# Performance work log

Hardware: AMD Instinct MI355X
Metric: run time of the kernel (lower is better)

## Reference

```python
import jax, jax.numpy as jnp
import numpy as np

N_NODES = 10000
N_EDGES = 640000
IN_CH = 128
OUT_CH = 128


def setup_inputs() -> dict:
    key = jax.random.key(0)
    k1, k2, k3, k4 = jax.random.split(key, 4)
    x = jax.random.normal(k1, (N_NODES, IN_CH), dtype=jnp.float32)
    edge_index = jax.random.randint(k2, (2, N_EDGES), 0, N_NODES, dtype=jnp.int64)
    # nn.Linear(2*in_channels, out_channels): weight [out, 2*in], bias [out]
    bound = 1.0 / np.sqrt(2 * IN_CH)
    W = jax.random.uniform(k3, (OUT_CH, 2 * IN_CH), dtype=jnp.float32, minval=-bound, maxval=bound)
    b = jax.random.uniform(k4, (OUT_CH,), dtype=jnp.float32, minval=-bound, maxval=bound)
    return {"x": x, "W": W, "b": b, "edge_index": edge_index}


def reference(x, W, b, edge_index):
    # PyG convention: edge_index[0] = source j, edge_index[1] = target i
    src, dst = edge_index[0], edge_index[1]
    x_i = x[dst]                      # [E, C] target features
    x_j = x[src]                      # [E, C] source features
    feat = jnp.concatenate([x_i, x_j - x_i], axis=-1)  # [E, 2C]
    msg = feat @ W.T + b              # [E, out]
    out = jax.ops.segment_max(msg, dst, num_segments=x.shape[0])  # [N, out]
    # isolated nodes: PyG scatter-max yields 0, segment_max yields -inf
    return jnp.where(jnp.isfinite(out), out, 0.0)
```

## Files before the change

### kernel.cpp

```cpp
#include <hip/hip_runtime.h>
#include <math.h>

#define N_CH 128
#define NB_MAX 512
#define BIN_CHUNK 4096
#define BIN_T 512

__global__ __launch_bounds__(256) void prep_kernel(const float* __restrict__ W,
                                                   float* __restrict__ V1,
                                                   float* __restrict__ V2,
                                                   int* __restrict__ binCount,
                                                   int nb) {
    int i = blockIdx.x * 256 + threadIdx.x;
    if (i < N_CH * N_CH) {
        int k = i >> 7, o = i & 127;
        float w1 = W[o * 256 + k];
        float w2 = W[o * 256 + 128 + k];
        V1[i] = w1 - w2;
        V2[i] = w2;
    }
    if (i < nb) binCount[i] = 0;
}

__global__ __launch_bounds__(256) void gemm_kernel(const float* __restrict__ x,
                                                   const float* __restrict__ V1,
                                                   const float* __restrict__ V2,
                                                   const float* __restrict__ bias,
                                                   float* __restrict__ A,
                                                   unsigned short* __restrict__ Bh,
                                                   int n_nodes) {
    __shared__ float xs[32][N_CH];
    const int n0 = blockIdx.x * 32;
    const int tid = threadIdx.x;

    if (n0 + 32 <= n_nodes) {
        const float4* xg = (const float4*)(x + (size_t)n0 * N_CH);
        float4* xsv = (float4*)&xs[0][0];
        #pragma unroll
        for (int i = 0; i < 4; ++i) xsv[tid + i * 256] = xg[tid + i * 256];
    } else {
        for (int i = tid; i < 32 * N_CH; i += 256) {
            int n = n0 + (i >> 7);
            (&xs[0][0])[i] = (n < n_nodes) ? x[(size_t)n * N_CH + (i & 127)] : 0.f;
        }
    }
    __syncthreads();

    const int o  = tid & 127;
    const int nh = tid >> 7;
    const float bo = bias[o];
    float acc1[16], acc2[16];
    #pragma unroll
    for (int i = 0; i < 16; ++i) { acc1[i] = 0.f; acc2[i] = 0.f; }

    const float* xrow = &xs[nh * 16][0];
    for (int k4 = 0; k4 < N_CH; k4 += 4) {
        float w1[4], w2[4];
        #pragma unroll
        for (int j = 0; j < 4; ++j) {
            w1[j] = V1[(k4 + j) * N_CH + o];
            w2[j] = V2[(k4 + j) * N_CH + o];
        }
        #pragma unroll
        for (int i = 0; i < 16; ++i) {
            float4 xv = *(const float4*)&xrow[i * N_CH + k4];
            acc1[i] = fmaf(xv.x, w1[0], acc1[i]); acc2[i] = fmaf(xv.x, w2[0], acc2[i]);
            acc1[i] = fmaf(xv.y, w1[1], acc1[i]); acc2[i] = fmaf(xv.y, w2[1], acc2[i]);
            acc1[i] = fmaf(xv.z, w1[2], acc1[i]); acc2[i] = fmaf(xv.z, w2[2], acc2[i]);
            acc1[i] = fmaf(xv.w, w1[3], acc1[i]); acc2[i] = fmaf(xv.w, w2[3], acc2[i]);
        }
    }

    #pragma unroll
    for (int i = 0; i < 16; ++i) {
        int n = n0 + nh * 16 + i;
        if (n < n_nodes) {
            A[(size_t)n * N_CH + o] = acc1[i] + bo;
            unsigned int bits = __float_as_uint(acc2[i]);
            unsigned int r = (bits + 0x7FFFu + ((bits >> 16) & 1u)) >> 16;
            Bh[(size_t)n * N_CH + o] = (unsigned short)r;
        }
    }
}

__global__ __launch_bounds__(256) void bhist_kernel(const int* __restrict__ dst,
                                                    int* __restrict__ binCount,
                                                    int n_edges, int nb) {
    __shared__ int h[NB_MAX];
    const int tid = threadIdx.x;
    for (int i = tid; i < nb; i += 256) h[i] = 0;
    __syncthreads();
    const int base = blockIdx.x * BIN_CHUNK;
    const int cnt = min(BIN_CHUNK, n_edges - base);
    for (int j = tid; j < cnt; j += 256)
        atomicAdd(&h[dst[base + j] >> 5], 1);
    __syncthreads();
    for (int i = tid; i < nb; i += 256)
        if (h[i]) atomicAdd(&binCount[i], h[i]);
}

__global__ __launch_bounds__(512) void bscan_kernel(const int* __restrict__ binCount,
                                                    int* __restrict__ binOff,
                                                    int* __restrict__ binCursor,
                                                    int nb) {
    __shared__ int t[512];
    const int tid = threadIdx.x;
    int v = (tid < nb) ? binCount[tid] : 0;
    t[tid] = v;
    __syncthreads();
    #pragma unroll
    for (int off = 1; off < 512; off <<= 1) {
        int u = (tid >= off) ? t[tid - off] : 0;
        __syncthreads();
        t[tid] += u;
        __syncthreads();
    }
    if (tid < nb) {
        int excl = t[tid] - v;
        binOff[tid] = excl;
        binCursor[tid] = excl;
    }
    if (tid == 0) binOff[nb] = t[nb - 1];
}

__global__ __launch_bounds__(BIN_T) void bin_kernel(const int* __restrict__ src,
                                                    const int* __restrict__ dst,
                                                    int* __restrict__ binCursor,
                                                    unsigned int* __restrict__ binned,
                                                    int n_edges, int nb) {
    __shared__ unsigned int   lpk[BIN_CHUNK];
    __shared__ unsigned short lbk[BIN_CHUNK];
    __shared__ int sc[512];
    __shared__ int lhist[NB_MAX], lexcl[NB_MAX], lcur[NB_MAX], bbase[NB_MAX];

    const int tid = threadIdx.x;
    const int base = blockIdx.x * BIN_CHUNK;
    const int cnt = min(BIN_CHUNK, n_edges - base);

    for (int i = tid; i < nb; i += BIN_T) lhist[i] = 0;
    __syncthreads();

    unsigned int vreg[BIN_CHUNK / BIN_T];
    unsigned short breg[BIN_CHUNK / BIN_T];
    int nloc = 0;
    for (int j = tid; j < cnt; j += BIN_T) {
        int s = src[base + j];
        int d = dst[base + j];
        int b = d >> 5;
        vreg[nloc] = ((unsigned int)(d & 31) << 14) | (unsigned int)s;
        breg[nloc] = (unsigned short)b;
        ++nloc;
        atomicAdd(&lhist[b], 1);
    }
    __syncthreads();

    int v = (tid < nb) ? lhist[tid] : 0;
    sc[tid] = v;
    __syncthreads();
    #pragma unroll
    for (int off = 1; off < 512; off <<= 1) {
        int u = (tid >= off) ? sc[tid - off] : 0;
        __syncthreads();
        sc[tid] += u;
        __syncthreads();
    }
    if (tid < nb) {
        int excl = sc[tid] - v;
        lexcl[tid] = excl;
        lcur[tid] = excl;
    }
    __syncthreads();

    for (int k = 0; k < nloc; ++k) {
        int b = breg[k];
        int p = atomicAdd(&lcur[b], 1);
        lpk[p] = vreg[k];
        lbk[p] = (unsigned short)b;
    }
    __syncthreads();

    for (int b = tid; b < nb; b += BIN_T) {
        int c = lhist[b];
        if (c) bbase[b] = atomicAdd(&binCursor[b], c);
    }
    __syncthreads();

    for (int i = tid; i < cnt; i += BIN_T) {
        int b = lbk[i];
        binned[bbase[b] + (i - lexcl[b])] = lpk[i];
    }
}

__global__ __launch_bounds__(256) void build_kernel(const unsigned int* __restrict__ binned,
                                                    const int* __restrict__ binOff,
                                                    int* __restrict__ offsets,
                                                    int* __restrict__ eidx,
                                                    int n_nodes, int nb) {
    __shared__ int lhist[32], lexcl[33], lcur[32];
    const int b = blockIdx.x;
    const int tid = threadIdx.x;
    const int rbeg = binOff[b], rend = binOff[b + 1];

    if (tid < 32) { lhist[tid] = 0; lcur[tid] = 0; }
    __syncthreads();
    for (int i = rbeg + tid; i < rend; i += 256)
        atomicAdd(&lhist[binned[i] >> 14], 1);
    __syncthreads();
    if (tid == 0) {
        int s = 0;
        for (int k = 0; k < 32; ++k) { lexcl[k] = s; s += lhist[k]; }
        lexcl[32] = s;
    }
    __syncthreads();
    if (tid < 32) {
        int n = b * 32 + tid;
        if (n < n_nodes) offsets[n] = rbeg + lexcl[tid];
    }
    if (b == nb - 1 && tid == 0) offsets[n_nodes] = rend;
    for (int i = rbeg + tid; i < rend; i += 256) {
        unsigned int w = binned[i];
        int d5 = (int)(w >> 14);
        int r = atomicAdd(&lcur[d5], 1);
        eidx[rbeg + lexcl[d5] + r] = (int)(w & 16383u);
    }
}

__global__ __launch_bounds__(256) void gather_kernel(
        const float* __restrict__ A,
        const unsigned int* __restrict__ Bh2,
        const int* __restrict__ offsets,
        const int* __restrict__ eidx,
        float* __restrict__ out,
        int n_nodes) {
    __shared__ int sidx[4][64];
    const int g = threadIdx.x >> 6;
    const int l = threadIdx.x & 63;
    const int n = blockIdx.x * 4 + g;
    if (n >= n_nodes) return;
    const int beg = offsets[n], end = offsets[n + 1];

    float mlo[8], mhi[8];
    #pragma unroll
    for (int i = 0; i < 8; ++i) { mlo[i] = -INFINITY; mhi[i] = -INFINITY; }

    for (int base = beg; base < end; base += 64) {
        int p = base + l;
        if (p < end) sidx[g][l] = eidx[p];
        int cnt = min(64, end - base);
        int q = 0;
        for (; q + 8 <= cnt; q += 8) {
            unsigned int w[8];
            #pragma unroll
            for (int i = 0; i < 8; ++i)
                w[i] = Bh2[(size_t)sidx[g][q + i] * 64 + l];
            #pragma unroll
            for (int i = 0; i < 8; ++i) {
                mlo[i] = fmaxf(mlo[i], __uint_as_float(w[i] << 16));
                mhi[i] = fmaxf(mhi[i], __uint_as_float(w[i] & 0xFFFF0000u));
            }
        }
        for (; q < cnt; ++q) {
            unsigned int w = Bh2[(size_t)sidx[g][q] * 64 + l];
            mlo[0] = fmaxf(mlo[0], __uint_as_float(w << 16));
            mhi[0] = fmaxf(mhi[0], __uint_as_float(w & 0xFFFF0000u));
        }
    }

    float lo = mlo[0], hi = mhi[0];
    #pragma unroll
    for (int i = 1; i < 8; ++i) { lo = fmaxf(lo, mlo[i]); hi = fmaxf(hi, mhi[i]); }

    float2 r = make_float2(0.f, 0.f);
    if (end > beg) {
        float2 a = *(const float2*)(A + (size_t)n * N_CH + 2 * l);
        r.x = a.x + lo;
        r.y = a.y + hi;
    }
    *(float2*)(out + (size_t)n * N_CH + 2 * l) = r;
}

extern "C" void kernel_launch(void* const* d_in, const int* in_sizes, int n_in,
                              void* d_out, int out_size, void* d_ws, size_t ws_size,
                              hipStream_t stream) {
    const float* x = (const float*)d_in[0];
    const float* W = (const float*)d_in[1];
    const float* b = (const float*)d_in[2];
    const int*   ei = (const int*)d_in[3];

    const int n_nodes = in_sizes[0] / N_CH;
    const int n_edges = in_sizes[3] / 2;
    const int nb = (n_nodes + 31) >> 5;
    const int* src = ei;
    const int* dst = ei + n_edges;
    float* out = (float*)d_out;

    char* ws = (char*)d_ws;
    size_t off = 0;
    auto alloc = [&](size_t bytes) -> void* {
        void* p = ws + off;
        off += (bytes + 255) & ~(size_t)255;
        return p;
    };
    float* V1        = (float*)alloc((size_t)N_CH * N_CH * 4);
    float* V2        = (float*)alloc((size_t)N_CH * N_CH * 4);
    float* A         = (float*)alloc((size_t)n_nodes * N_CH * 4);
    unsigned short* Bh = (unsigned short*)alloc((size_t)n_nodes * N_CH * 2);
    int*   binCount  = (int*)alloc((size_t)nb * 4);
    int*   binOff    = (int*)alloc((size_t)(nb + 1) * 4);
    int*   binCursor = (int*)alloc((size_t)nb * 4);
    unsigned int* binned = (unsigned int*)alloc((size_t)n_edges * 4);
    int*   offsets   = (int*)alloc((size_t)(n_nodes + 1) * 4);
    int*   eidx      = (int*)alloc((size_t)n_edges * 4);
    (void)ws_size; (void)n_in; (void)out_size;

    const int nbin_blocks = (n_edges + BIN_CHUNK - 1) / BIN_CHUNK;

    prep_kernel <<<(N_CH * N_CH + 255) / 256, 256, 0, stream>>>(W, V1, V2, binCount, nb);
    gemm_kernel <<<(n_nodes + 31) / 32, 256, 0, stream>>>(x, V1, V2, b, A, Bh, n_nodes);
    bhist_kernel<<<nbin_blocks, 256, 0, stream>>>(dst, binCount, n_edges, nb);
    bscan_kernel<<<1, 512, 0, stream>>>(binCount, binOff, binCursor, nb);
    bin_kernel  <<<nbin_blocks, BIN_T, 0, stream>>>(src, dst, binCursor, binned, n_edges, nb);
    build_kernel<<<nb, 256, 0, stream>>>(binned, binOff, offsets, eidx, n_nodes, nb);
    gather_kernel<<<(n_nodes + 3) / 4, 256, 0, stream>>>(A, (const unsigned int*)Bh, offsets, eidx, out, n_nodes);
}
```

Before: 138.5 us.

## Replace global bin-cursor atomics with per-block histograms and in-block scans

The W-prep and the bin histogram are merged into one kernel that writes per-block bin counts, so the separate global histogram and scan kernels go away. The bin kernel now gets each block's global offsets by summing the per-block counts itself and running warp-shuffle scans. This gives a deterministic, stable ordering and drops the global cursor atomics. Packing the full destination into the binned word removes the separate bin-id array, loads are vectorised as int4, and the build kernel uses per-wave histograms to cut LDS atomic contention. In exchange, every bin block redundantly reads all nblk×nb counts (about 157×313 ints).

```diff
diff --git a/kernel.cpp b/kernel.cpp
--- a/kernel.cpp
+++ b/kernel.cpp
@@ -6,20 +6,67 @@
 #define BIN_CHUNK 4096
 #define BIN_T 512
 
-__global__ __launch_bounds__(256) void prep_kernel(const float* __restrict__ W,
-                                                   float* __restrict__ V1,
-                                                   float* __restrict__ V2,
-                                                   int* __restrict__ binCount,
-                                                   int nb) {
-    int i = blockIdx.x * 256 + threadIdx.x;
-    if (i < N_CH * N_CH) {
-        int k = i >> 7, o = i & 127;
-        float w1 = W[o * 256 + k];
-        float w2 = W[o * 256 + 128 + k];
-        V1[i] = w1 - w2;
-        V2[i] = w2;
-    }
-    if (i < nb) binCount[i] = 0;
+__device__ __forceinline__ int block_excl_scan512(int v, int tid, int* wsums) {
+    __syncthreads();
+    const int lane = tid & 63, w = tid >> 6;
+    int inc = v;
+    #pragma unroll
+    for (int i = 1; i < 64; i <<= 1) {
+        int t = __shfl_up(inc, i, 64);
+        if (lane >= i) inc += t;
+    }
+    if (lane == 63) wsums[w] = inc;
+    __syncthreads();
+    if (w == 0) {
+        int s = (lane < 8) ? wsums[lane] : 0;
+        #pragma unroll
+        for (int i = 1; i < 8; i <<= 1) {
+            int t = __shfl_up(s, i, 64);
+            if (lane >= i) s += t;
+        }
+        if (lane < 8) wsums[lane] = s;
+    }
+    __syncthreads();
+    int base = (w > 0) ? wsums[w - 1] : 0;
+    return base + inc - v;
+}
+
+__global__ __launch_bounds__(BIN_T) void preph_kernel(const float* __restrict__ W,
+                                                      const int* __restrict__ dst,
+                                                      float* __restrict__ V1,
+                                                      float* __restrict__ V2,
+                                                      int* __restrict__ binCountPB,
+                                                      int n_edges, int nb, int nblk) {
+    const int tid = threadIdx.x;
+    if ((int)blockIdx.x == nblk) {
+        for (int i = tid; i < N_CH * N_CH; i += BIN_T) {
+            int k = i >> 7, o = i & 127;
+            float w1 = W[o * 256 + k];
+            float w2 = W[o * 256 + 128 + k];
+            V1[i] = w1 - w2;
+            V2[i] = w2;
+        }
+        return;
+    }
+    __shared__ int h[NB_MAX];
+    for (int i = tid; i < nb; i += BIN_T) h[i] = 0;
+    __syncthreads();
+    const int base = blockIdx.x * BIN_CHUNK;
+    const int cnt = min(BIN_CHUNK, n_edges - base);
+    for (int j0 = tid * 4; j0 < cnt; j0 += BIN_T * 4) {
+        if (j0 + 3 < cnt) {
+            int4 d = *(const int4*)(dst + base + j0);
+            atomicAdd(&h[d.x >> 5], 1);
+            atomicAdd(&h[d.y >> 5], 1);
+            atomicAdd(&h[d.z >> 5], 1);
+            atomicAdd(&h[d.w >> 5], 1);
+        } else {
+            for (int j = j0; j < cnt; ++j) atomicAdd(&h[dst[base + j] >> 5], 1);
+        }
+    }
+    __syncthreads();
+    for (int i = tid; i < nb; i += BIN_T)
+        binCountPB[blockIdx.x * nb + i] = h[i];
 }
 
 __global__ __launch_bounds__(256) void gemm_kernel(const float* __restrict__ x,
@@ -83,111 +130,73 @@
     }
 }
 
-__global__ __launch_bounds__(256) void bhist_kernel(const int* __restrict__ dst,
-                                                    int* __restrict__ binCount,
-                                                    int n_edges, int nb) {
-    __shared__ int h[NB_MAX];
-    const int tid = threadIdx.x;
-    for (int i = tid; i < nb; i += 256) h[i] = 0;
-    __syncthreads();
-    const int base = blockIdx.x * BIN_CHUNK;
-    const int cnt = min(BIN_CHUNK, n_edges - base);
-    for (int j = tid; j < cnt; j += 256)
-        atomicAdd(&h[dst[base + j] >> 5], 1);
-    __syncthreads();
-    for (int i = tid; i < nb; i += 256)
-        if (h[i]) atomicAdd(&binCount[i], h[i]);
-}
-
-__global__ __launch_bounds__(512) void bscan_kernel(const int* __restrict__ binCount,
-                                                    int* __restrict__ binOff,
-                                                    int* __restrict__ binCursor,
-                                                    int nb) {
-    __shared__ int t[512];
-    const int tid = threadIdx.x;
-    int v = (tid < nb) ? binCount[tid] : 0;
-    t[tid] = v;
-    __syncthreads();
-    #pragma unroll
-    for (int off = 1; off < 512; off <<= 1) {
-        int u = (tid >= off) ? t[tid - off] : 0;
-        __syncthreads();
-        t[tid] += u;
-        __syncthreads();
-    }
-    if (tid < nb) {
-        int excl = t[tid] - v;
-        binOff[tid] = excl;
-        binCursor[tid] = excl;
-    }
-    if (tid == 0) binOff[nb] = t[nb - 1];
-}
-
 __global__ __launch_bounds__(BIN_T) void bin_kernel(const int* __restrict__ src,
                                                     const int* __restrict__ dst,
-                                                    int* __restrict__ binCursor,
+                                                    const int* __restrict__ binCountPB,
+                                                    int* __restrict__ binOff,
                                                     unsigned int* __restrict__ binned,
-                                                    int n_edges, int nb) {
-    __shared__ unsigned int   lpk[BIN_CHUNK];
-    __shared__ unsigned short lbk[BIN_CHUNK];
-    __shared__ int sc[512];
-    __shared__ int lhist[NB_MAX], lexcl[NB_MAX], lcur[NB_MAX], bbase[NB_MAX];
+                                                    int n_edges, int nb, int nblk) {
+    __shared__ unsigned int lpk[BIN_CHUNK];
+    __shared__ int gbase[NB_MAX];
+    __shared__ int lexcl[NB_MAX];
+    __shared__ int lcur[NB_MAX];
+    __shared__ int gOff[NB_MAX];
+    __shared__ int wsums[8];
 
     const int tid = threadIdx.x;
-    const int base = blockIdx.x * BIN_CHUNK;
+    const int bid = blockIdx.x;
+    const int base = bid * BIN_CHUNK;
     const int cnt = min(BIN_CHUNK, n_edges - base);
 
-    for (int i = tid; i < nb; i += BIN_T) lhist[i] = 0;
-    __syncthreads();
+    int tot = 0, pre = 0, own = 0;
+    if (tid < nb) {
+        for (int j = 0; j < nblk; ++j) {
+            int c = binCountPB[j * nb + tid];
+            tot += c;
+            if (j < bid) pre += c;
+            if (j == bid) own = c;
+        }
+    }
+    int offT = block_excl_scan512(tot, tid, wsums);
+    if (tid < nb) gOff[tid] = offT;
+    int offO = block_excl_scan512(own, tid, wsums);
+    if (tid < nb) {
+        lexcl[tid] = offO;
+        lcur[tid] = offO;
+        gbase[tid] = offT + pre;
+    }
+    if (bid == 0 && tid == 0) binOff[nb] = n_edges;
+    __syncthreads();
+    if (bid == 0) {
+        for (int i = tid; i < nb; i += BIN_T) binOff[i] = gOff[i];
+    }
 
     unsigned int vreg[BIN_CHUNK / BIN_T];
-    unsigned short breg[BIN_CHUNK / BIN_T];
     int nloc = 0;
-    for (int j = tid; j < cnt; j += BIN_T) {
-        int s = src[base + j];
-        int d = dst[base + j];
-        int b = d >> 5;
-        vreg[nloc] = ((unsigned int)(d & 31) << 14) | (unsigned int)s;
-        breg[nloc] = (unsigned short)b;
-        ++nloc;
-        atomicAdd(&lhist[b], 1);
-    }
-    __syncthreads();
-
-    int v = (tid < nb) ? lhist[tid] : 0;
-    sc[tid] = v;
-    __syncthreads();
-    #pragma unroll
-    for (int off = 1; off < 512; off <<= 1) {
-        int u = (tid >= off) ? sc[tid - off] : 0;
-        __syncthreads();
-        sc[tid] += u;
-        __syncthreads();
-    }
-    if (tid < nb) {
-        int excl = sc[tid] - v;
-        lexcl[tid] = excl;
-        lcur[tid] = excl;
-    }
-    __syncthreads();
-
+    for (int j0 = tid * 4; j0 < cnt; j0 += BIN_T * 4) {
+        if (j0 + 3 < cnt) {
+            int4 s4 = *(const int4*)(src + base + j0);
+            int4 d4 = *(const int4*)(dst + base + j0);
+            vreg[nloc++] = ((unsigned int)d4.x << 14) | (unsigned int)s4.x;
+            vreg[nloc++] = ((unsigned int)d4.y << 14) | (unsigned int)s4.y;
+            vreg[nloc++] = ((unsigned int)d4.z << 14) | (unsigned int)s4.z;
+            vreg[nloc++] = ((unsigned int)d4.w << 14) | (unsigned int)s4.w;
+        } else {
+            for (int j = j0; j < cnt; ++j)
+                vreg[nloc++] = ((unsigned int)dst[base + j] << 14) | (unsigned int)src[base + j];
+        }
+    }
     for (int k = 0; k < nloc; ++k) {
-        int b = breg[k];
+        int b = (int)(vreg[k] >> 19);
         int p = atomicAdd(&lcur[b], 1);
         lpk[p] = vreg[k];
-        lbk[p] = (unsigned short)b;
-    }
-    __syncthreads();
-
-    for (int b = tid; b < nb; b += BIN_T) {
-        int c = lhist[b];
-        if (c) bbase[b] = atomicAdd(&binCursor[b], c);
     }
     __syncthreads();
 
     for (int i = tid; i < cnt; i += BIN_T) {
-        int b = lbk[i];
-        binned[bbase[b] + (i - lexcl[b])] = lpk[i];
+        unsigned int w = lpk[i];
+        int b = (int)(w >> 19);
+        binned[gbase[b] + (i - lexcl[b])] = w;
     }
 }
 
@@ -196,32 +205,46 @@
                                                     int* __restrict__ offsets,
                                                     int* __restrict__ eidx,
                                                     int n_nodes, int nb) {
-    __shared__ int lhist[32], lexcl[33], lcur[32];
+    __shared__ int whist[4][32];
+    __shared__ int lexcl[33];
     const int b = blockIdx.x;
     const int tid = threadIdx.x;
+    const int w = tid >> 6;
     const int rbeg = binOff[b], rend = binOff[b + 1];
 
-    if (tid < 32) { lhist[tid] = 0; lcur[tid] = 0; }
+    if (tid < 128) ((int*)whist)[tid] = 0;
     __syncthreads();
     for (int i = rbeg + tid; i < rend; i += 256)
-        atomicAdd(&lhist[binned[i] >> 14], 1);
+        atomicAdd(&whist[w][(binned[i] >> 14) & 31], 1);
     __syncthreads();
     if (tid == 0) {
         int s = 0;
-        for (int k = 0; k < 32; ++k) { lexcl[k] = s; s += lhist[k]; }
+        #pragma unroll
+        for (int k = 0; k < 32; ++k) {
+            lexcl[k] = s;
+            s += whist[0][k] + whist[1][k] + whist[2][k] + whist[3][k];
+        }
         lexcl[32] = s;
     }
     __syncthreads();
     if (tid < 32) {
+        int basec = lexcl[tid];
+        #pragma unroll
+        for (int ww = 0; ww < 4; ++ww) {
+            int c = whist[ww][tid];
+            whist[ww][tid] = basec;
+            basec += c;
+        }
         int n = b * 32 + tid;
         if (n < n_nodes) offsets[n] = rbeg + lexcl[tid];
     }
     if (b == nb - 1 && tid == 0) offsets[n_nodes] = rend;
+    __syncthreads();
     for (int i = rbeg + tid; i < rend; i += 256) {
-        unsigned int w = binned[i];
-        int d5 = (int)(w >> 14);
-        int r = atomicAdd(&lcur[d5], 1);
-        eidx[rbeg + lexcl[d5] + r] = (int)(w & 16383u);
+        unsigned int wd = binned[i];
+        int v = (int)((wd >> 14) & 31);
+        int r = atomicAdd(&whist[w][v], 1);
+        eidx[rbeg + r] = (int)(wd & 16383u);
     }
 }
 
@@ -301,25 +324,22 @@
         off += (bytes + 255) & ~(size_t)255;
         return p;
     };
-    float* V1        = (float*)alloc((size_t)N_CH * N_CH * 4);
-    float* V2        = (float*)alloc((size_t)N_CH * N_CH * 4);
-    float* A         = (float*)alloc((size_t)n_nodes * N_CH * 4);
+    const int nblk = (n_edges + BIN_CHUNK - 1) / BIN_CHUNK;
+
+    float* V1          = (float*)alloc((size_t)N_CH * N_CH * 4);
+    float* V2          = (float*)alloc((size_t)N_CH * N_CH * 4);
+    float* A           = (float*)alloc((size_t)n_nodes * N_CH * 4);
     unsigned short* Bh = (unsigned short*)alloc((size_t)n_nodes * N_CH * 2);
-    int*   binCount  = (int*)alloc((size_t)nb * 4);
-    int*   binOff    = (int*)alloc((size_t)(nb + 1) * 4);
-    int*   binCursor = (int*)alloc((size_t)nb * 4);
+    int* binCountPB    = (int*)alloc((size_t)nblk * nb * 4);
+    int* binOff        = (int*)alloc((size_t)(nb + 1) * 4);
     unsigned int* binned = (unsigned int*)alloc((size_t)n_edges * 4);
-    int*   offsets   = (int*)alloc((size_t)(n_nodes + 1) * 4);
-    int*   eidx      = (int*)alloc((size_t)n_edges * 4);
+    int* offsets       = (int*)alloc((size_t)(n_nodes + 1) * 4);
+    int* eidx          = (int*)alloc((size_t)n_edges * 4);
     (void)ws_size; (void)n_in; (void)out_size;
 
-    const int nbin_blocks = (n_edges + BIN_CHUNK - 1) / BIN_CHUNK;
-
-    prep_kernel <<<(N_CH * N_CH + 255) / 256, 256, 0, stream>>>(W, V1, V2, binCount, nb);
+    preph_kernel<<<nblk + 1, BIN_T, 0, stream>>>(W, dst, V1, V2, binCountPB, n_edges, nb, nblk);
     gemm_kernel <<<(n_nodes + 31) / 32, 256, 0, stream>>>(x, V1, V2, b, A, Bh, n_nodes);
-    bhist_kernel<<<nbin_blocks, 256, 0, stream>>>(dst, binCount, n_edges, nb);
-    bscan_kernel<<<1, 512, 0, stream>>>(binCount, binOff, binCursor, nb);
-    bin_kernel  <<<nbin_blocks, BIN_T, 0, stream>>>(src, dst, binCursor, binned, n_edges, nb);
+    bin_kernel  <<<nblk, BIN_T, 0, stream>>>(src, dst, binCountPB, binOff, binned, n_edges, nb, nblk);
     build_kernel<<<nb, 256, 0, stream>>>(binned, binOff, offsets, eidx, n_nodes, nb);
     gather_kernel<<<(n_nodes + 3) / 4, 256, 0, stream>>>(A, (const unsigned int*)Bh, offsets, eidx, out, n_nodes);
 }
```

Measured after the change: 178.6 us. +29.0%, slower.
